# Optimization experiments

Hardware: AMD Instinct MI355X
Metric: run time of the kernel (lower is better)

Reference implementation:

```python
import jax, jax.numpy as jnp
import numpy as np

B, S, W = 128, 100, 20
D, L, H, DFF = 192, 6, 8, 256
DH = D // H

def _ln(x, g, b, eps=1e-5):
    m = jnp.mean(x, -1, keepdims=True)
    v = jnp.var(x, -1, keepdims=True)
    return (x - m) * jax.lax.rsqrt(v + eps) * g + b

def _pos_encoding(seq_len, d):
    pos = np.arange(seq_len, dtype=np.float32)[:, None]
    div = np.exp(np.arange(0, d, 2, dtype=np.float32) * (-np.log(10000.0) / d))
    pe = np.zeros((seq_len, d), dtype=np.float32)
    pe[:, 0::2] = np.sin(pos * div)
    pe[:, 1::2] = np.cos(pos * div)
    return jnp.asarray(pe)

def setup_inputs() -> dict:
    key = jax.random.key(0)
    ks = iter(jax.random.split(key, 80))
    def nrm(shape, s=0.05):
        return jax.random.normal(next(ks), shape, jnp.float32) * s
    inp = {
        'title_idx': jax.random.randint(next(ks), (B, S, W), 0, 1000),
        'class_idx': jax.random.randint(next(ks), (B, S, W), 0, 500),
        'process_idx': jax.random.randint(next(ks), (B, S, W), 0, 1000),
        'activity_type': jax.random.randint(next(ks), (B, S), 0, 4),
        'mouse_pos': jax.random.uniform(next(ks), (B, S, 2), jnp.float32),
        'rect': jax.random.uniform(next(ks), (B, S, W, 4), jnp.float32),
        'flags': jax.random.uniform(next(ks), (B, S, W, 2), jnp.float32),
        'keyboard_active': jax.random.uniform(next(ks), (B, S, 1), jnp.float32),
        'window_mask': jnp.ones((B, S, W), jnp.float32),
        'noise': jax.random.normal(next(ks), (W, B, D), jnp.float32),
        'title_emb': nrm((1000, 32)),
        'class_emb': nrm((500, 32)),
        'process_emb': nrm((1000, 32)),
        'spatial_w1': nrm((64, 6)), 'spatial_b1': nrm((64,)),
        'spatial_w2': nrm((32, 64)), 'spatial_b2': nrm((32,)),
        'wfuse_w': nrm((128, 128)), 'wfuse_b': nrm((128,)),
        'mouse_w1': nrm((32, 2)), 'mouse_b1': nrm((32,)),
        'mouse_w2': nrm((32, 32)), 'mouse_b2': nrm((32,)),
        'act_emb': nrm((4, 16)),
        'kbd_w': nrm((16, 1)), 'kbd_b': nrm((16,)),
        'afuse_w': nrm((64, 64)), 'afuse_b': nrm((64,)),
        'qkv_w': nrm((L, 3 * D, D)), 'qkv_b': nrm((L, 3 * D)),
        'out_w': nrm((L, D, D)), 'out_b': nrm((L, D)),
        'ff1_w': nrm((L, DFF, D)), 'ff1_b': nrm((L, DFF)),
        'ff2_w': nrm((L, D, DFF)), 'ff2_b': nrm((L, D)),
        'ln1_g': 1.0 + nrm((L, D)), 'ln1_b': nrm((L, D)),
        'ln2_g': 1.0 + nrm((L, D)), 'ln2_b': nrm((L, D)),
        'proj_w1': nrm((256, 192)), 'proj_b1': nrm((256,)),
        'proj_w2': nrm((4, 256)), 'proj_b2': nrm((4,)),
        'ex_w1': nrm((128, 192)), 'ex_b1': nrm((128,)),
        'ex_w2': nrm((1, 128)), 'ex_b2': nrm((1,)),
    }
    return inp

def reference(title_idx, class_idx, process_idx, activity_type, mouse_pos, rect, flags, keyboard_active, window_mask, noise, title_emb, class_emb, process_emb, spatial_w1, spatial_b1, spatial_w2, spatial_b2, wfuse_w, wfuse_b, mouse_w1, mouse_b1, mouse_w2, mouse_b2, act_emb, kbd_w, kbd_b, afuse_w, afuse_b, qkv_w, qkv_b, out_w, out_b, ff1_w, ff1_b, ff2_w, ff2_b, ln1_g, ln1_b, ln2_g, ln2_b, proj_w1, proj_b1, proj_w2, proj_b2, ex_w1, ex_b1, ex_w2, ex_b2):
    # ---- window feature extraction (vectorized over B,S,W) ----
    t = title_emb[title_idx]              # [B,S,W,32]
    c = class_emb[class_idx]
    p = process_emb[process_idx]
    sp_in = jnp.concatenate([rect, flags], -1)  # [B,S,W,6]
    sp = jax.nn.relu(sp_in @ spatial_w1.T + spatial_b1) @ spatial_w2.T + spatial_b2
    wcomb = jnp.concatenate([t, c, p, sp], -1)  # [B,S,W,128]
    wf = jax.nn.relu(wcomb @ wfuse_w.T + wfuse_b) * window_mask[..., None]
    avg_w = jnp.sum(wf, 2) / W            # mean over max_windows incl zero padding
    # ---- activity feature extraction ----
    mp = mouse_pos / jnp.array([1920.0, 1080.0], jnp.float32)
    mf = jax.nn.relu(mp @ mouse_w1.T + mouse_b1) @ mouse_w2.T + mouse_b2  # [B,S,32]
    ae = act_emb[activity_type]           # [B,S,16]
    kf = keyboard_active @ kbd_w.T + kbd_b  # [B,S,16]
    af = jax.nn.relu(jnp.concatenate([mf, ae, kf], -1) @ afuse_w.T + afuse_b)
    # ---- transformer ----
    x = jnp.concatenate([avg_w, af], -1) + _pos_encoding(S, D)[None]  # [B,S,192]
    scale = 1.0 / np.sqrt(DH)
    def block(h, prm):
        qw, qb, ow, ob, f1w, f1b, f2w, f2b, g1, b1, g2, b2 = prm
        qkv = h @ qw.T + qb
        q, k, v = jnp.split(qkv, 3, -1)
        q = q.reshape(B, S, H, DH); k = k.reshape(B, S, H, DH); v = v.reshape(B, S, H, DH)
        a = jax.nn.softmax(jnp.einsum('bqhd,bkhd->bhqk', q, k) * scale, -1)
        o = jnp.einsum('bhqk,bkhd->bqhd', a, v).reshape(B, S, D)
        h = _ln(h + o @ ow.T + ob, g1, b1)
        ff = jax.nn.relu(h @ f1w.T + f1b) @ f2w.T + f2b
        return _ln(h + ff, g2, b2), None
    x, _ = jax.lax.scan(block, x, (qkv_w, qkv_b, out_w, out_b, ff1_w, ff1_b, ff2_w, ff2_b, ln1_g, ln1_b, ln2_g, ln2_b))
    last = x[:, -1, :]                    # [B,192]
    # ---- per-slot heads (noise passed in deterministically) ----
    slot = last[None] + noise * 0.1       # [W,B,192]
    positions = jnp.transpose(jax.nn.relu(slot @ proj_w1.T + proj_b1) @ proj_w2.T + proj_b2, (1, 0, 2))  # [B,W,4]
    existence = jnp.transpose(jax.nn.sigmoid(jax.nn.relu(slot @ ex_w1.T + ex_b1) @ ex_w2.T + ex_b2)[..., 0], (1, 0))  # [B,W]
    return positions, existence
```

## Files before the change

### kernel.cpp

```cpp
#include <hip/hip_runtime.h>
#include <hip/hip_bf16.h>
#include <math.h>

#define B_ 128
#define S_ 100
#define W_ 20
#define D_ 192
#define L_ 6
#define H_ 8
#define DFF_ 256
#define DH_ 24
#define BS_ (B_*S_)
#define THREED_ 576

typedef short short8 __attribute__((ext_vector_type(8)));
typedef short short4v __attribute__((ext_vector_type(4)));
typedef float floatx16 __attribute__((ext_vector_type(16)));

__device__ __forceinline__ float posenc(int s, int c) {
  float freq = expf(-logf(10000.f) * (float)(2 * (c >> 1)) / (float)D_);
  float ang = (float)s * freq;
  return (c & 1) ? cosf(ang) : sinf(ang);
}

__device__ __forceinline__ short8 ld_frag8(const __hip_bfloat16* p) {
  short4v lo = *(const short4v*)p;
  short4v hi = *(const short4v*)(p + 4);
  short8 r;
  r[0]=lo[0]; r[1]=lo[1]; r[2]=lo[2]; r[3]=lo[3];
  r[4]=hi[0]; r[5]=hi[1]; r[6]=hi[2]; r[7]=hi[3];
  return r;
}

__device__ __forceinline__ short f2bf_s(float v) {
  __hip_bfloat16 t = __float2bfloat16(v);
  return *reinterpret_cast<short*>(&t);
}

__device__ __forceinline__ float dot4(float4 a, float4 b) {
  return a.x*b.x + a.y*b.y + a.z*b.z + a.w*b.w;
}

__global__ __launch_bounds__(256)
void convertprep_kernel(
    const float* __restrict__ s0, __hip_bfloat16* __restrict__ d0,
    const float* __restrict__ s1, __hip_bfloat16* __restrict__ d1,
    const float* __restrict__ s2, __hip_bfloat16* __restrict__ d2,
    const float* __restrict__ s3, __hip_bfloat16* __restrict__ d3,
    const float* __restrict__ te, const float* __restrict__ ce,
    const float* __restrict__ pe, const float* __restrict__ wfw,
    const float* __restrict__ wfb, const float* __restrict__ sw2,
    const float* __restrict__ sb2,
    float* __restrict__ TE2, float* __restrict__ CE2,
    float* __restrict__ PE2, __hip_bfloat16* __restrict__ WSPb,
    float* __restrict__ PEtab)
{
  int b = blockIdx.x, tid = threadIdx.x;
  if (b < 720) {
    const float* s; __hip_bfloat16* d; int base;
    if      (b < 324) { s = s0; d = d0; base = b; }
    else if (b < 432) { s = s1; d = d1; base = b - 324; }
    else if (b < 576) { s = s2; d = d2; base = b - 432; }
    else              { s = s3; d = d3; base = b - 576; }
    int i = (base * 256 + tid) * 8;
    float4 v0 = *(const float4*)(s + i);
    float4 v1 = *(const float4*)(s + i + 4);
    __hip_bfloat162* d2p = (__hip_bfloat162*)(d + i);
    d2p[0] = __float22bfloat162_rn(make_float2(v0.x, v0.y));
    d2p[1] = __float22bfloat162_rn(make_float2(v0.z, v0.w));
    d2p[2] = __float22bfloat162_rn(make_float2(v1.x, v1.y));
    d2p[3] = __float22bfloat162_rn(make_float2(v1.z, v1.w));
    return;
  }
  int blk = b - 720;
  if (blk < 1250) {
    int item = blk * 256 + tid;
    int v = item >> 7, o = item & 127;
    const float* src; float* dst; int base, vv;
    float a;
    if (v < 1000) {
      src = te; dst = TE2; base = 0; vv = v;
      a = wfb[o];
      const float4* w4 = (const float4*)(wfw + o * 128 + 96);
      const float4* b4 = (const float4*)sb2;
      #pragma unroll
      for (int k4 = 0; k4 < 8; ++k4) a += dot4(w4[k4], b4[k4]);
    } else if (v < 1500) {
      src = ce; dst = CE2; base = 32; vv = v - 1000; a = 0.f;
    } else {
      src = pe; dst = PE2; base = 64; vv = v - 1500; a = 0.f;
    }
    const float4* s4 = (const float4*)(src + vv * 32);
    const float4* w4 = (const float4*)(wfw + o * 128 + base);
    #pragma unroll
    for (int k4 = 0; k4 < 8; ++k4) a += dot4(s4[k4], w4[k4]);
    int op = ((o & 31) << 2) + (o >> 5);
    dst[vv * 128 + op] = a;
  } else if (blk < 1282) {
    int item = (blk - 1250) * 256 + tid;
    int j = item >> 7, o = item & 127;
    float a = 0.f;
    #pragma unroll 8
    for (int k = 0; k < 32; ++k) a += wfw[o * 128 + 96 + k] * sw2[k * 64 + j];
    WSPb[o * 64 + j] = __float2bfloat16(a);
  } else {
    int idx = (blk - 1282) * 256 + tid;
    int s_ = idx / D_, c = idx - s_ * D_;
    PEtab[idx] = posenc(s_, c);
  }
}

__global__ __launch_bounds__(512)
void encode8_kernel(
    const int* __restrict__ title_idx, const int* __restrict__ class_idx,
    const int* __restrict__ process_idx, const int* __restrict__ activity_type,
    const float* __restrict__ mouse_pos, const float* __restrict__ rect,
    const float* __restrict__ flags, const float* __restrict__ keyboard_active,
    const float* __restrict__ window_mask,
    const float* __restrict__ sw1, const float* __restrict__ sb1,
    const float* __restrict__ TE2, const float* __restrict__ CE2,
    const float* __restrict__ PE2, const __hip_bfloat16* __restrict__ WSPb,
    const float* __restrict__ PEtab,
    const float* __restrict__ mw1, const float* __restrict__ mb1,
    const float* __restrict__ mw2, const float* __restrict__ mb2,
    const float* __restrict__ act_emb, const float* __restrict__ kbw,
    const float* __restrict__ kbb,
    const float* __restrict__ afw, const float* __restrict__ afb,
    float* __restrict__ x, __hip_bfloat16* __restrict__ xb)
{
  __shared__ __hip_bfloat16 Bls[128][72];
  __shared__ int   idxS[8][20][3];
  __shared__ float maskS[8][20];
  __shared__ __align__(16) float rectS[8][20][8];

  int tid = threadIdx.x;
  int w = tid >> 6, lane = tid & 63;
  int m32 = lane & 31, half = lane >> 5;
  int bs0 = blockIdx.x * 8;
  int bs = bs0 + w;

  if (tid < 480) {
    int g2 = tid / 60, rem = tid % 60, which = rem / 20, w_ = rem % 20;
    const int* src = (which == 0) ? title_idx : (which == 1) ? class_idx : process_idx;
    idxS[g2][w_][which] = src[(bs0 + g2) * W_ + w_];
  }
  if (tid < 160) {
    int g2 = tid / 20, w_ = tid % 20;
    maskS[g2][w_] = window_mask[(bs0 + g2) * W_ + w_];
  }
  for (int e = tid; e < 960; e += 512) {
    int g2 = e / 120, rem = e % 120, w_ = rem / 6, c = rem % 6;
    int rg = (bs0 + g2) * W_ + w_;
    rectS[g2][w_][c] = (c < 4) ? rect[rg * 4 + c] : flags[rg * 2 + (c - 4)];
  }
  for (int e = tid; e < 1024; e += 512) {
    int col = e >> 3, k8 = e & 7;
    short8 v = *(const short8*)&WSPb[col * 64 + k8 * 8];
    *(short8*)&Bls[col][k8 * 8] = v;
  }
  __syncthreads();

  short8 afr[4];
  {
    float rc[6];
    bool act = (m32 < W_);
    if (act) {
      #pragma unroll
      for (int c = 0; c < 6; ++c) rc[c] = rectS[w][m32][c];
    }
    #pragma unroll
    for (int s = 0; s < 4; ++s) {
      short8 f;
      #pragma unroll
      for (int jp = 0; jp < 8; ++jp) {
        float a = 0.f;
        if (act) {
          int j = s * 16 + half * 8 + jp;
          const float* w1 = sw1 + j * 6;
          a = sb1[j];
          #pragma unroll
          for (int c = 0; c < 6; ++c) a += w1[c] * rc[c];
          a = fmaxf(a, 0.f);
        }
        f[jp] = f2bf_s(a);
      }
      afr[s] = f;
    }
  }

  floatx16 acc[4];
  #pragma unroll
  for (int nt = 0; nt < 4; ++nt)
    #pragma unroll
    for (int r = 0; r < 16; ++r) acc[nt][r] = 0.f;

  #pragma unroll
  for (int s = 0; s < 4; ++s) {
    int ko = s * 16 + half * 8;
    #pragma unroll
    for (int nt = 0; nt < 4; ++nt) {
      short8 bf = *(const short8*)&Bls[nt * 32 + m32][ko];
      acc[nt] = __builtin_amdgcn_mfma_f32_32x32x16_bf16(afr[s], bf, acc[nt], 0, 0, 0);
    }
  }

  float cs[4] = {0.f, 0.f, 0.f, 0.f};
  #pragma unroll
  for (int r = 0; r < 16; ++r) {
    int row = (r & 3) + 8 * (r >> 2) + 4 * half;
    if (row < W_) {
      int t  = idxS[w][row][0];
      int ci = idxS[w][row][1];
      int p  = idxS[w][row][2];
      float mk = maskS[w][row];
      float4 gt = *(const float4*)&TE2[(size_t)t  * 128 + m32 * 4];
      float4 gc = *(const float4*)&CE2[(size_t)ci * 128 + m32 * 4];
      float4 gp = *(const float4*)&PE2[(size_t)p  * 128 + m32 * 4];
      float g0 = gt.x + gc.x + gp.x;
      float g1 = gt.y + gc.y + gp.y;
      float g2v = gt.z + gc.z + gp.z;
      float g3 = gt.w + gc.w + gp.w;
      cs[0] += fmaxf(acc[0][r] + g0, 0.f) * mk;
      cs[1] += fmaxf(acc[1][r] + g1, 0.f) * mk;
      cs[2] += fmaxf(acc[2][r] + g2v, 0.f) * mk;
      cs[3] += fmaxf(acc[3][r] + g3, 0.f) * mk;
    }
  }
  #pragma unroll
  for (int nt = 0; nt < 4; ++nt) cs[nt] += __shfl_xor(cs[nt], 32);
  if (half == 0) {
    int s_ = bs % S_;
    #pragma unroll
    for (int nt = 0; nt < 4; ++nt) {
      int col = nt * 32 + m32;
      float v = cs[nt] * (1.f / (float)W_) + PEtab[s_ * D_ + col];
      x[(size_t)bs * D_ + col] = v;
      xb[(size_t)bs * D_ + col] = __float2bfloat16(v);
    }
  }

  {
    float* wsc = &rectS[w][0][0];
    if (lane < 32) {
      float mx = mouse_pos[bs * 2 + 0] * (1.f / 1920.f);
      float my = mouse_pos[bs * 2 + 1] * (1.f / 1080.f);
      wsc[64 + lane] = fmaxf(mw1[lane * 2] * mx + mw1[lane * 2 + 1] * my + mb1[lane], 0.f);
    }
    __builtin_amdgcn_wave_barrier();
    float cv;
    if (lane < 32) {
      float a = mb2[lane];
      const float4* wv = (const float4*)(mw2 + lane * 32);
      const float4* hv = (const float4*)(wsc + 64);
      #pragma unroll
      for (int k4 = 0; k4 < 8; ++k4) {
        float4 ww = wv[k4], hh = hv[k4];
        a += ww.x*hh.x + ww.y*hh.y + ww.z*hh.z + ww.w*hh.w;
      }
      cv = a;
    } else if (lane < 48) {
      cv = act_emb[activity_type[bs] * 16 + (lane - 32)];
    } else {
      cv = kbw[lane - 48] * keyboard_active[bs] + kbb[lane - 48];
    }
    wsc[lane] = cv;
    __builtin_amdgcn_wave_barrier();
    {
      float a = afb[lane];
      const float4* w4 = (const float4*)(afw + lane * 64);
      const float4* cp = (const float4*)wsc;
      #pragma unroll
      for (int k4 = 0; k4 < 16; ++k4) {
        float4 ww = w4[k4], c2 = cp[k4];
        a += ww.x*c2.x + ww.y*c2.y + ww.z*c2.z + ww.w*c2.w;
      }
      float v = fmaxf(a, 0.f);
      int cg = 128 + lane;
      float ovv = v + PEtab[(bs % S_) * D_ + cg];
      x[(size_t)bs * D_ + cg] = ovv;
      xb[(size_t)bs * D_ + cg] = __float2bfloat16(ovv);
    }
  }
}

__global__ __launch_bounds__(256)
void qkvattn_kernel(const __hip_bfloat16* __restrict__ xb,
                    const __hip_bfloat16* __restrict__ Wq,
                    const float* __restrict__ qb,
                    __hip_bfloat16* __restrict__ o)
{
  __shared__ __align__(16) char smem[40960];
  __hip_bfloat16* Asl = (__hip_bfloat16*)smem;
  __hip_bfloat16* Bsl = (__hip_bfloat16*)(smem + 18432);
  __hip_bfloat16* Qs  = (__hip_bfloat16*)smem;
  __hip_bfloat16* Ks  = (__hip_bfloat16*)(smem + 10240);
  __hip_bfloat16* Ps  = (__hip_bfloat16*)smem;
  __hip_bfloat16* Vt  = (__hip_bfloat16*)(smem + 33792);

  int bh = blockIdx.x;
  int hh = bh & 7, b = bh >> 3;
  int tid = threadIdx.x, lane = tid & 63, w = tid >> 6;
  int m32 = lane & 31, half = lane >> 5;

  for (int e = tid; e < (32 * 112) / 8; e += 256)
    ((float4*)Vt)[e] = make_float4(0.f, 0.f, 0.f, 0.f);

  int rA0 = tid >> 2,          hA0 = tid & 3;
  int rA1 = (tid + 256) >> 2,  hA1 = tid & 3;
  int rrA0 = rA0 < S_ ? rA0 : S_ - 1;
  int rrA1 = rA1 < S_ ? rA1 : S_ - 1;
  size_t baseA0 = (size_t)(b * S_ + rrA0) * D_;
  size_t baseA1 = (size_t)(b * S_ + rrA1) * D_;
  float4* dA0 = (float4*)&Asl[rA0 * 72 + hA0 * 16];
  float4* dA1 = (float4*)&Asl[rA1 * 72 + hA1 * 16];

  int rB0 = tid >> 2, hB0 = tid & 3;
  int tB0 = rB0 >> 5, jB0 = rB0 & 31;
  bool actB0 = (jB0 < DH_);
  bool isB1 = (tid < 128);
  int rB1 = (tid + 256) >> 2, hB1 = tid & 3;
  int tB1 = rB1 >> 5, jB1 = rB1 & 31;
  bool actB1 = isB1 && (jB1 < DH_);
  size_t baseB0 = actB0 ? (size_t)(tB0 * D_ + hh * DH_ + jB0) * D_ : 0;
  size_t baseB1 = actB1 ? (size_t)(tB1 * D_ + hh * DH_ + jB1) * D_ : 0;
  float4* dB0 = (float4*)&Bsl[rB0 * 72 + hB0 * 16];
  float4* dB1 = (float4*)&Bsl[rB1 * 72 + hB1 * 16];

  {
    float4 z = make_float4(0.f, 0.f, 0.f, 0.f);
    if (!actB0) { dB0[0] = z; dB0[1] = z; }
    if (isB1 && !actB1) { dB1[0] = z; dB1[1] = z; }
  }
  {
    const float4* s0 = (const float4*)&xb[baseA0 + hA0 * 16];
    float4 a00 = s0[0], a01 = s0[1];
    const float4* s1 = (const float4*)&xb[baseA1 + hA1 * 16];
    float4 a10 = s1[0], a11 = s1[1];
    if (actB0) {
      const float4* p = (const float4*)&Wq[baseB0 + hB0 * 16];
      dB0[0] = p[0]; dB0[1] = p[1];
    }
    if (actB1) {
      const float4* p = (const float4*)&Wq[baseB1 + hB1 * 16];
      dB1[0] = p[0]; dB1[1] = p[1];
    }
    dA0[0] = a00; dA0[1] = a01;
    dA1[0] = a10; dA1[1] = a11;
  }

  floatx16 acc[3];
  #pragma unroll
  for (int t = 0; t < 3; ++t)
    #pragma unroll
    for (int r = 0; r < 16; ++r) acc[t][r] = 0.f;

  for (int k0 = 0; k0 < D_; k0 += 64) {
    bool more = (k0 + 64 < D_);
    __syncthreads();
    float4 a00, a01, a10, a11, b00, b01, b10, b11;
    if (more) {
      const float4* s0 = (const float4*)&xb[baseA0 + k0 + 64 + hA0 * 16];
      a00 = s0[0]; a01 = s0[1];
      const float4* s1 = (const float4*)&xb[baseA1 + k0 + 64 + hA1 * 16];
      a10 = s1[0]; a11 = s1[1];
      if (actB0) {
        const float4* p = (const float4*)&Wq[baseB0 + k0 + 64 + hB0 * 16];
        b00 = p[0]; b01 = p[1];
      }
      if (actB1) {
        const float4* p = (const float4*)&Wq[baseB1 + k0 + 64 + hB1 * 16];
        b10 = p[0]; b11 = p[1];
      }
    }
    #pragma unroll
    for (int kc = 0; kc < 4; ++kc) {
      int ko = kc * 16 + half * 8;
      short8 a = *(const short8*)&Asl[(w * 32 + m32) * 72 + ko];
      #pragma unroll
      for (int t = 0; t < 3; ++t) {
        short8 bf = *(const short8*)&Bsl[(t * 32 + m32) * 72 + ko];
        acc[t] = __builtin_amdgcn_mfma_f32_32x32x16_bf16(a, bf, acc[t], 0, 0, 0);
      }
    }
    __syncthreads();
    if (more) {
      dA0[0] = a00; dA0[1] = a01;
      dA1[0] = a10; dA1[1] = a11;
      if (actB0) { dB0[0] = b00; dB0[1] = b01; }
      if (actB1) { dB1[0] = b10; dB1[1] = b11; }
    }
  }
  {
    bool dv = (m32 < DH_);
    float bq = dv ? qb[0 * D_ + hh * DH_ + m32] : 0.f;
    float bk = dv ? qb[1 * D_ + hh * DH_ + m32] : 0.f;
    float bv = dv ? qb[2 * D_ + hh * DH_ + m32] : 0.f;
    #pragma unroll
    for (int r = 0; r < 16; ++r) {
      int row = w * 32 + (r & 3) + 8 * (r >> 2) + 4 * half;
      Qs[row * 40 + m32] = __float2bfloat16(dv ? acc[0][r] + bq : 0.f);
      Ks[row * 40 + m32] = __float2bfloat16(dv ? acc[1][r] + bk : 0.f);
      if (dv && row < S_) Vt[m32 * 112 + row] = __float2bfloat16(acc[2][r] + bv);
    }
  }
  __syncthreads();

  floatx16 sc[4];
  #pragma unroll
  for (int nt = 0; nt < 4; ++nt)
    #pragma unroll
    for (int r = 0; r < 16; ++r) sc[nt][r] = 0.f;
  #pragma unroll
  for (int kc = 0; kc < 2; ++kc) {
    int ko = kc * 16 + half * 8;
    short8 a = *(const short8*)&Qs[(w * 32 + m32) * 40 + ko];
    #pragma unroll
    for (int nt = 0; nt < 4; ++nt) {
      short8 bf = *(const short8*)&Ks[(nt * 32 + m32) * 40 + ko];
      sc[nt] = __builtin_amdgcn_mfma_f32_32x32x16_bf16(a, bf, sc[nt], 0, 0, 0);
    }
  }
  __syncthreads();

  const float scale = 0.20412414523193154f;
  float rinv[16];
  #pragma unroll
  for (int r = 0; r < 16; ++r) {
    float mx = -1e30f;
    #pragma unroll
    for (int nt = 0; nt < 4; ++nt) {
      float s = sc[nt][r] * scale;
      if (nt == 3 && m32 >= 4) s = -1e30f;
      sc[nt][r] = s;
      mx = fmaxf(mx, s);
    }
    #pragma unroll
    for (int off = 1; off < 32; off <<= 1) mx = fmaxf(mx, __shfl_xor(mx, off));
    float sum = 0.f;
    #pragma unroll
    for (int nt = 0; nt < 4; ++nt) {
      float e = expf(sc[nt][r] - mx);
      sc[nt][r] = e;
      sum += e;
    }
    #pragma unroll
    for (int off = 1; off < 32; off <<= 1) sum += __shfl_xor(sum, off);
    rinv[r] = 1.f / sum;
  }
  #pragma unroll
  for (int r = 0; r < 16; ++r) {
    int rowl = (r & 3) + 8 * (r >> 2) + 4 * half;
    #pragma unroll
    for (int nt = 0; nt < 4; ++nt)
      Ps[(w * 32 + rowl) * 132 + nt * 32 + m32] = __float2bfloat16(sc[nt][r]);
  }

  floatx16 ov;
  #pragma unroll
  for (int r = 0; r < 16; ++r) ov[r] = 0.f;
  #pragma unroll
  for (int kt = 0; kt < 7; ++kt) {
    int ko = kt * 16 + half * 8;
    short8 a = ld_frag8(&Ps[(w * 32 + m32) * 132 + ko]);
    short8 bf = *(const short8*)&Vt[m32 * 112 + ko];
    ov = __builtin_amdgcn_mfma_f32_32x32x16_bf16(a, bf, ov, 0, 0, 0);
  }
  #pragma unroll
  for (int r = 0; r < 16; ++r) {
    int rowl = (r & 3) + 8 * (r >> 2) + 4 * half;
    int q = w * 32 + rowl;
    if (m32 < DH_ && q < S_)
      o[((size_t)(b * S_ + q)) * D_ + hh * DH_ + m32] =
          __float2bfloat16(ov[r] * rinv[r]);
  }
}

__global__ __launch_bounds__(256)
void outffln_kernel(const __hip_bfloat16* __restrict__ attb,
                    const __hip_bfloat16* __restrict__ Wo, const float* __restrict__ bo,
                    const float* __restrict__ g1, const float* __restrict__ b1v,
                    const __hip_bfloat16* __restrict__ W1, const float* __restrict__ b1,
                    const __hip_bfloat16* __restrict__ W2, const float* __restrict__ b2,
                    const float* __restrict__ g2, const float* __restrict__ b2v,
                    float* __restrict__ x, __hip_bfloat16* __restrict__ xb)
{
  __shared__ __align__(16) char arena[61952];
  __hip_bfloat16* AslA  = (__hip_bfloat16*)arena;
  __hip_bfloat16* BslA  = (__hip_bfloat16*)(arena + 9216);
  __hip_bfloat16* Afull = (__hip_bfloat16*)arena;
  __hip_bfloat16* BslB1 = (__hip_bfloat16*)(arena + 25088);
  __hip_bfloat16* C1    = (__hip_bfloat16*)arena;
  __hip_bfloat16* BslB2 = (__hip_bfloat16*)(arena + 33280);
  float (*psum)[2] = (float(*)[2])(arena + 60928);
  float (*psq)[2]  = (float(*)[2])(arena + 61440);

  int tid = threadIdx.x, lane = tid & 63, w = tid >> 6;
  int m32 = lane & 31, half = lane >> 5;
  int mt = w & 1, ng = w >> 1;
  int bm = blockIdx.x * 64;

  floatx16 accA[3];
  #pragma unroll
  for (int j = 0; j < 3; ++j)
    #pragma unroll
    for (int r = 0; r < 16; ++r) accA[j][r] = 0.f;

  {
    int ra = tid >> 2, ha = tid & 3;
    float4* dA = (float4*)&AslA[ra * 72 + ha * 16];
    int rb0 = tid >> 2,           hb0 = tid & 3;
    int rb1 = (tid + 256) >> 2,   hb1 = tid & 3;
    int rb2 = (tid + 512) >> 2,   hb2 = tid & 3;
    float4* dB0 = (float4*)&BslA[rb0 * 72 + hb0 * 16];
    float4* dB1 = (float4*)&BslA[rb1 * 72 + hb1 * 16];
    float4* dB2 = (float4*)&BslA[rb2 * 72 + hb2 * 16];

    {
      const float4* s = (const float4*)(attb + (size_t)(bm + ra) * D_ + ha * 16);
      dA[0] = s[0]; dA[1] = s[1];
      const float4* p0 = (const float4*)(Wo + (size_t)rb0 * D_ + hb0 * 16);
      dB0[0] = p0[0]; dB0[1] = p0[1];
      const float4* p1 = (const float4*)(Wo + (size_t)rb1 * D_ + hb1 * 16);
      dB1[0] = p1[0]; dB1[1] = p1[1];
      const float4* p2 = (const float4*)(Wo + (size_t)rb2 * D_ + hb2 * 16);
      dB2[0] = p2[0]; dB2[1] = p2[1];
    }
    for (int k0 = 0; k0 < D_; k0 += 64) {
      bool more = (k0 + 64 < D_);
      __syncthreads();
      float4 na0, na1, n00, n01, n10, n11, n20, n21;
      if (more) {
        const float4* s = (const float4*)(attb + (size_t)(bm + ra) * D_ + k0 + 64 + ha * 16);
        na0 = s[0]; na1 = s[1];
        const float4* p0 = (const float4*)(Wo + (size_t)rb0 * D_ + k0 + 64 + hb0 * 16);
        n00 = p0[0]; n01 = p0[1];
        const float4* p1 = (const float4*)(Wo + (size_t)rb1 * D_ + k0 + 64 + hb1 * 16);
        n10 = p1[0]; n11 = p1[1];
        const float4* p2 = (const float4*)(Wo + (size_t)rb2 * D_ + k0 + 64 + hb2 * 16);
        n20 = p2[0]; n21 = p2[1];
      }
      #pragma unroll
      for (int kc = 0; kc < 4; ++kc) {
        int ko = kc * 16 + half * 8;
        short8 a = *(const short8*)&AslA[(mt * 32 + m32) * 72 + ko];
        #pragma unroll
        for (int j = 0; j < 3; ++j) {
          short8 bf = *(const short8*)&BslA[((ng * 3 + j) * 32 + m32) * 72 + ko];
          accA[j] = __builtin_amdgcn_mfma_f32_32x32x16_bf16(a, bf, accA[j], 0, 0, 0);
        }
      }
      __syncthreads();
      if (more) {
        dA[0] = na0; dA[1] = na1;
        dB0[0] = n00; dB0[1] = n01;
        dB1[0] = n10; dB1[1] = n11;
        dB2[0] = n20; dB2[1] = n21;
      }
    }
  }
  {
    int rowb = mt * 32 + 4 * half;
    #pragma unroll
    for (int r = 0; r < 16; ++r) {
      int rl = rowb + (r & 3) + 8 * (r >> 2);
      int row = bm + rl;
      float p = 0.f;
      #pragma unroll
      for (int j = 0; j < 3; ++j) {
        int col = (ng * 3 + j) * 32 + m32;
        float t = accA[j][r] + bo[col] + x[(size_t)row * D_ + col];
        accA[j][r] = t;
        p += t;
      }
      #pragma unroll
      for (int off = 1; off < 32; off <<= 1) p += __shfl_xor(p, off);
      if (m32 == 0) psum[rl][ng] = p;
    }
    __syncthreads();
    float mean[16];
    #pragma unroll
    for (int r = 0; r < 16; ++r) {
      int rl = rowb + (r & 3) + 8 * (r >> 2);
      mean[r] = (psum[rl][0] + psum[rl][1]) * (1.f / (float)D_);
    }
    #pragma unroll
    for (int r = 0; r < 16; ++r) {
      int rl = rowb + (r & 3) + 8 * (r >> 2);
      float s = 0.f;
      #pragma unroll
      for (int j = 0; j < 3; ++j) { float dd = accA[j][r] - mean[r]; s += dd * dd; }
      #pragma unroll
      for (int off = 1; off < 32; off <<= 1) s += __shfl_xor(s, off);
      if (m32 == 0) psq[rl][ng] = s;
    }
    __syncthreads();
    #pragma unroll
    for (int r = 0; r < 16; ++r) {
      int rl = rowb + (r & 3) + 8 * (r >> 2);
      int row = bm + rl;
      float inv = rsqrtf((psq[rl][0] + psq[rl][1]) * (1.f / (float)D_) + 1e-5f);
      #pragma unroll
      for (int j = 0; j < 3; ++j) {
        int col = (ng * 3 + j) * 32 + m32;
        float ovv = (accA[j][r] - mean[r]) * inv * g1[col] + b1v[col];
        x[(size_t)row * D_ + col] = ovv;
        __hip_bfloat16 hb = __float2bfloat16(ovv);
        xb[(size_t)row * D_ + col] = hb;
        Afull[rl * 196 + col] = hb;
      }
    }
  }
  __syncthreads();

  floatx16 acc1[4];
  #pragma unroll
  for (int j = 0; j < 4; ++j)
    #pragma unroll
    for (int r = 0; r < 16; ++r) acc1[j][r] = 0.f;

  {
    int rb0 = tid >> 2,          hb0 = tid & 3;
    int rb1 = (tid + 256) >> 2,  hb1 = tid & 3;
    int rb2 = (tid + 512) >> 2,  hb2 = tid & 3;
    int rb3 = (tid + 768) >> 2,  hb3 = tid & 3;
    float4* dB0 = (float4*)&BslB1[rb0 * 72 + hb0 * 16];
    float4* dB1 = (float4*)&BslB1[rb1 * 72 + hb1 * 16];
    float4* dB2 = (float4*)&BslB1[rb2 * 72 + hb2 * 16];
    float4* dB3 = (float4*)&BslB1[rb3 * 72 + hb3 * 16];
    {
      const float4* p0 = (const float4*)(W1 + (size_t)rb0 * D_ + hb0 * 16);
      dB0[0] = p0[0]; dB0[1] = p0[1];
      const float4* p1 = (const float4*)(W1 + (size_t)rb1 * D_ + hb1 * 16);
      dB1[0] = p1[0]; dB1[1] = p1[1];
      const float4* p2 = (const float4*)(W1 + (size_t)rb2 * D_ + hb2 * 16);
      dB2[0] = p2[0]; dB2[1] = p2[1];
      const float4* p3 = (const float4*)(W1 + (size_t)rb3 * D_ + hb3 * 16);
      dB3[0] = p3[0]; dB3[1] = p3[1];
    }
    for (int k0 = 0; k0 < D_; k0 += 64) {
      bool more = (k0 + 64 < D_);
      __syncthreads();
      float4 n00, n01, n10, n11, n20, n21, n30, n31;
      if (more) {
        const float4* p0 = (const float4*)(W1 + (size_t)rb0 * D_ + k0 + 64 + hb0 * 16);
        n00 = p0[0]; n01 = p0[1];
        const float4* p1 = (const float4*)(W1 + (size_t)rb1 * D_ + k0 + 64 + hb1 * 16);
        n10 = p1[0]; n11 = p1[1];
        const float4* p2 = (const float4*)(W1 + (size_t)rb2 * D_ + k0 + 64 + hb2 * 16);
        n20 = p2[0]; n21 = p2[1];
        const float4* p3 = (const float4*)(W1 + (size_t)rb3 * D_ + k0 + 64 + hb3 * 16);
        n30 = p3[0]; n31 = p3[1];
      }
      #pragma unroll
      for (int kc = 0; kc < 4; ++kc) {
        int ko = kc * 16 + half * 8;
        short8 a = ld_frag8(&Afull[(mt * 32 + m32) * 196 + k0 + ko]);
        #pragma unroll
        for (int j = 0; j < 4; ++j) {
          short8 bf = *(const short8*)&BslB1[((ng * 4 + j) * 32 + m32) * 72 + ko];
          acc1[j] = __builtin_amdgcn_mfma_f32_32x32x16_bf16(a, bf, acc1[j], 0, 0, 0);
        }
      }
      __syncthreads();
      if (more) {
        dB0[0] = n00; dB0[1] = n01;
        dB1[0] = n10; dB1[1] = n11;
        dB2[0] = n20; dB2[1] = n21;
        dB3[0] = n30; dB3[1] = n31;
      }
    }
  }
  {
    int rowb = mt * 32 + 4 * half;
    #pragma unroll
    for (int j = 0; j < 4; ++j) {
      int col = (ng * 4 + j) * 32 + m32;
      float cb = b1[col];
      #pragma unroll
      for (int r = 0; r < 16; ++r) {
        int row = rowb + (r & 3) + 8 * (r >> 2);
        C1[row * 260 + col] = __float2bfloat16(fmaxf(acc1[j][r] + cb, 0.f));
      }
    }
  }

  floatx16 acc2[3];
  #pragma unroll
  for (int j = 0; j < 3; ++j)
    #pragma unroll
    for (int r = 0; r < 16; ++r) acc2[j][r] = 0.f;

  {
    int rb0 = tid >> 2,          hb0 = tid & 3;
    int rb1 = (tid + 256) >> 2,  hb1 = tid & 3;
    int rb2 = (tid + 512) >> 2,  hb2 = tid & 3;
    float4* dB0 = (float4*)&BslB2[rb0 * 72 + hb0 * 16];
    float4* dB1 = (float4*)&BslB2[rb1 * 72 + hb1 * 16];
    float4* dB2 = (float4*)&BslB2[rb2 * 72 + hb2 * 16];
    {
      const float4* p0 = (const float4*)(W2 + (size_t)rb0 * DFF_ + hb0 * 16);
      dB0[0] = p0[0]; dB0[1] = p0[1];
      const float4* p1 = (const float4*)(W2 + (size_t)rb1 * DFF_ + hb1 * 16);
      dB1[0] = p1[0]; dB1[1] = p1[1];
      const float4* p2 = (const float4*)(W2 + (size_t)rb2 * DFF_ + hb2 * 16);
      dB2[0] = p2[0]; dB2[1] = p2[1];
    }
    for (int k0 = 0; k0 < DFF_; k0 += 64) {
      bool more = (k0 + 64 < DFF_);
      __syncthreads();
      float4 n00, n01, n10, n11, n20, n21;
      if (more) {
        const float4* p0 = (const float4*)(W2 + (size_t)rb0 * DFF_ + k0 + 64 + hb0 * 16);
        n00 = p0[0]; n01 = p0[1];
        const float4* p1 = (const float4*)(W2 + (size_t)rb1 * DFF_ + k0 + 64 + hb1 * 16);
        n10 = p1[0]; n11 = p1[1];
        const float4* p2 = (const float4*)(W2 + (size_t)rb2 * DFF_ + k0 + 64 + hb2 * 16);
        n20 = p2[0]; n21 = p2[1];
      }
      #pragma unroll
      for (int kc = 0; kc < 4; ++kc) {
        int ko = kc * 16 + half * 8;
        short8 a = ld_frag8(&C1[(mt * 32 + m32) * 260 + k0 + ko]);
        #pragma unroll
        for (int j = 0; j < 3; ++j) {
          short8 bf = *(const short8*)&BslB2[((ng * 3 + j) * 32 + m32) * 72 + ko];
          acc2[j] = __builtin_amdgcn_mfma_f32_32x32x16_bf16(a, bf, acc2[j], 0, 0, 0);
        }
      }
      __syncthreads();
      if (more) {
        dB0[0] = n00; dB0[1] = n01;
        dB1[0] = n10; dB1[1] = n11;
        dB2[0] = n20; dB2[1] = n21;
      }
    }
  }

  int rowb = mt * 32 + 4 * half;
  #pragma unroll
  for (int r = 0; r < 16; ++r) {
    int rl = rowb + (r & 3) + 8 * (r >> 2);
    int row = bm + rl;
    float p = 0.f;
    #pragma unroll
    for (int j = 0; j < 3; ++j) {
      int col = (ng * 3 + j) * 32 + m32;
      float t = acc2[j][r] + b2[col] + x[(size_t)row * D_ + col];
      acc2[j][r] = t;
      p += t;
    }
    #pragma unroll
    for (int off = 1; off < 32; off <<= 1) p += __shfl_xor(p, off);
    if (m32 == 0) psum[rl][ng] = p;
  }
  __syncthreads();
  float mean[16];
  #pragma unroll
  for (int r = 0; r < 16; ++r) {
    int rl = rowb + (r & 3) + 8 * (r >> 2);
    mean[r] = (psum[rl][0] + psum[rl][1]) * (1.f / (float)D_);
  }
  #pragma unroll
  for (int r = 0; r < 16; ++r) {
    int rl = rowb + (r & 3) + 8 * (r >> 2);
    float s = 0.f;
    #pragma unroll
    for (int j = 0; j < 3; ++j) { float dd = acc2[j][r] - mean[r]; s += dd * dd; }
    #pragma unroll
    for (int off = 1; off < 32; off <<= 1) s += __shfl_xor(s, off);
    if (m32 == 0) psq[rl][ng] = s;
  }
  __syncthreads();
  #pragma unroll
  for (int r = 0; r < 16; ++r) {
    int rl = rowb + (r & 3) + 8 * (r >> 2);
    int row = bm + rl;
    float inv = rsqrtf((psq[rl][0] + psq[rl][1]) * (1.f / (float)D_) + 1e-5f);
    #pragma unroll
    for (int j = 0; j < 3; ++j) {
      int col = (ng * 3 + j) * 32 + m32;
      float ovv = (acc2[j][r] - mean[r]) * inv * g2[col] + b2v[col];
      x[(size_t)row * D_ + col] = ovv;
      xb[(size_t)row * D_ + col] = __float2bfloat16(ovv);
    }
  }
}

__global__ __launch_bounds__(256)
void head3_kernel(const float* __restrict__ x, const float* __restrict__ noise,
                  const float* __restrict__ pw1, const float* __restrict__ pb1,
                  const float* __restrict__ pw2, const float* __restrict__ pb2,
                  const float* __restrict__ ew1, const float* __restrict__ eb1,
                  const float* __restrict__ ew2, const float* __restrict__ eb2,
                  float* __restrict__ out)
{
  __shared__ float slotS[4][192];
  __shared__ float phS[4][256];
  __shared__ float ehS[4][128];
  int blk = blockIdx.x;
  int b = blk / 5, g = blk - b * 5;
  int tid = threadIdx.x;

  const float* lastrow = x + ((size_t)b * S_ + (S_ - 1)) * D_;
  for (int e = tid; e < 4 * 192; e += 256) {
    int wl = e / 192, c = e - wl * 192;
    int wg = g * 4 + wl;
    slotS[wl][c] = lastrow[c] + noise[((size_t)wg * B_ + b) * D_ + c] * 0.1f;
  }
  __syncthreads();

  bool doe = (tid < 128);
  float accp[4], acce[4];
  {
    float bp = pb1[tid];
    float be = doe ? eb1[tid] : 0.f;
    #pragma unroll
    for (int wl = 0; wl < 4; ++wl) { accp[wl] = bp; acce[wl] = be; }
  }
  {
    const float4* wr = (const float4*)(pw1 + (size_t)tid * D_);
    const float4* we = (const float4*)(ew1 + (size_t)(doe ? tid : 0) * D_);
    for (int k4 = 0; k4 < 48; ++k4) {
      float4 wv = wr[k4];
      float4 ev = we[k4];
      #pragma unroll
      for (int wl = 0; wl < 4; ++wl) {
        float4 sv = *(const float4*)&slotS[wl][k4 * 4];
        accp[wl] += wv.x*sv.x + wv.y*sv.y + wv.z*sv.z + wv.w*sv.w;
        if (doe) acce[wl] += ev.x*sv.x + ev.y*sv.y + ev.z*sv.z + ev.w*sv.w;
      }
    }
  }
  #pragma unroll
  for (int wl = 0; wl < 4; ++wl) {
    phS[wl][tid] = fmaxf(accp[wl], 0.f);
    if (doe) ehS[wl][tid] = fmaxf(acce[wl], 0.f);
  }
  __syncthreads();

  if (tid < 16) {
    int wl = tid >> 2, c = tid & 3;
    float a = pb2[c];
    const float4* wr = (const float4*)(pw2 + c * 256);
    const float4* pp = (const float4*)&phS[wl][0];
    for (int k = 0; k < 64; ++k) {
      float4 wv = wr[k], pv = pp[k];
      a += wv.x*pv.x + wv.y*pv.y + wv.z*pv.z + wv.w*pv.w;
    }
    out[((size_t)b * W_ + g * 4 + wl) * 4 + c] = a;
  } else if (tid >= 64 && tid < 68) {
    int wl = tid - 64;
    float a = eb2[0];
    const float4* wr = (const float4*)ew2;
    const float4* pp = (const float4*)&ehS[wl][0];
    for (int k = 0; k < 32; ++k) {
      float4 wv = wr[k], pv = pp[k];
      a += wv.x*pv.x + wv.y*pv.y + wv.z*pv.z + wv.w*pv.w;
    }
    out[(size_t)B_ * W_ * 4 + (size_t)b * W_ + g * 4 + wl] = 1.f / (1.f + expf(-a));
  }
}

extern "C" void kernel_launch(void* const* d_in, const int* in_sizes, int n_in,
                              void* d_out, int out_size, void* d_ws, size_t ws_size,
                              hipStream_t stream)
{
  const int*   title_idx       = (const int*)  d_in[0];
  const int*   class_idx       = (const int*)  d_in[1];
  const int*   process_idx     = (const int*)  d_in[2];
  const int*   activity_type   = (const int*)  d_in[3];
  const float* mouse_pos       = (const float*)d_in[4];
  const float* rect            = (const float*)d_in[5];
  const float* flags           = (const float*)d_in[6];
  const float* keyboard_active = (const float*)d_in[7];
  const float* window_mask     = (const float*)d_in[8];
  const float* noise           = (const float*)d_in[9];
  const float* title_emb       = (const float*)d_in[10];
  const float* class_emb       = (const float*)d_in[11];
  const float* process_emb     = (const float*)d_in[12];
  const float* spatial_w1      = (const float*)d_in[13];
  const float* spatial_b1      = (const float*)d_in[14];
  const float* spatial_w2      = (const float*)d_in[15];
  const float* spatial_b2      = (const float*)d_in[16];
  const float* wfuse_w         = (const float*)d_in[17];
  const float* wfuse_b         = (const float*)d_in[18];
  const float* mouse_w1        = (const float*)d_in[19];
  const float* mouse_b1        = (const float*)d_in[20];
  const float* mouse_w2        = (const float*)d_in[21];
  const float* mouse_b2        = (const float*)d_in[22];
  const float* act_emb         = (const float*)d_in[23];
  const float* kbd_w           = (const float*)d_in[24];
  const float* kbd_b           = (const float*)d_in[25];
  const float* afuse_w         = (const float*)d_in[26];
  const float* afuse_b         = (const float*)d_in[27];
  const float* qkv_w           = (const float*)d_in[28];
  const float* qkv_b           = (const float*)d_in[29];
  const float* out_w           = (const float*)d_in[30];
  const float* out_b           = (const float*)d_in[31];
  const float* ff1_w           = (const float*)d_in[32];
  const float* ff1_b           = (const float*)d_in[33];
  const float* ff2_w           = (const float*)d_in[34];
  const float* ff2_b           = (const float*)d_in[35];
  const float* ln1_g           = (const float*)d_in[36];
  const float* ln1_b           = (const float*)d_in[37];
  const float* ln2_g           = (const float*)d_in[38];
  const float* ln2_b           = (const float*)d_in[39];
  const float* proj_w1         = (const float*)d_in[40];
  const float* proj_b1         = (const float*)d_in[41];
  const float* proj_w2         = (const float*)d_in[42];
  const float* proj_b2         = (const float*)d_in[43];
  const float* ex_w1           = (const float*)d_in[44];
  const float* ex_b1           = (const float*)d_in[45];
  const float* ex_w2           = (const float*)d_in[46];
  const float* ex_b2           = (const float*)d_in[47];

  float* out = (float*)d_out;

  float* x = (float*)d_ws;
  __hip_bfloat16* xb   = (__hip_bfloat16*)(x + (size_t)BS_ * D_);
  __hip_bfloat16* attb = xb   + (size_t)BS_ * D_;
  __hip_bfloat16* wqb  = attb + (size_t)BS_ * D_;
  __hip_bfloat16* wob  = wqb  + (size_t)L_ * THREED_ * D_;
  __hip_bfloat16* wf1b = wob  + (size_t)L_ * D_ * D_;
  __hip_bfloat16* wf2b = wf1b + (size_t)L_ * DFF_ * D_;
  float* TE2  = (float*)(wf2b + (size_t)L_ * D_ * DFF_);
  float* CE2  = TE2  + 1000 * 128;
  float* PE2  = CE2  + 500 * 128;
  __hip_bfloat16* WSPb = (__hip_bfloat16*)(PE2 + 1000 * 128);
  float* PEtab = (float*)(WSPb + 128 * 64);
  (void)ws_size; (void)n_in; (void)in_sizes; (void)out_size;

  convertprep_kernel<<<2077, 256, 0, stream>>>(
      qkv_w, wqb, out_w, wob, ff1_w, wf1b, ff2_w, wf2b,
      title_emb, class_emb, process_emb, wfuse_w, wfuse_b,
      spatial_w2, spatial_b2, TE2, CE2, PE2, WSPb, PEtab);

  encode8_kernel<<<BS_ / 8, 512, 0, stream>>>(
      title_idx, class_idx, process_idx, activity_type, mouse_pos, rect, flags,
      keyboard_active, window_mask, spatial_w1, spatial_b1,
      TE2, CE2, PE2, WSPb, PEtab,
      mouse_w1, mouse_b1, mouse_w2, mouse_b2, act_emb, kbd_w, kbd_b,
      afuse_w, afuse_b, x, xb);

  for (int l = 0; l < L_; ++l) {
    qkvattn_kernel<<<B_ * H_, 256, 0, stream>>>(
        xb, wqb + (size_t)l * THREED_ * D_, qkv_b + (size_t)l * THREED_, attb);
    outffln_kernel<<<BS_ / 64, 256, 0, stream>>>(
        attb, wob + (size_t)l * D_ * D_, out_b + (size_t)l * D_,
        ln1_g + (size_t)l * D_, ln1_b + (size_t)l * D_,
        wf1b + (size_t)l * DFF_ * D_, ff1_b + (size_t)l * DFF_,
        wf2b + (size_t)l * D_ * DFF_, ff2_b + (size_t)l * D_,
        ln2_g + (size_t)l * D_, ln2_b + (size_t)l * D_, x, xb);
  }

  head3_kernel<<<B_ * 5, 256, 0, stream>>>(
      x, noise, proj_w1, proj_b1, proj_w2, proj_b2,
      ex_w1, ex_b1, ex_w2, ex_b2, out);
}
```

Before: 657.0 us.

## Widen out-proj K tile to 96 and keep residuals in registers

The out-projection GEMM in the fused out/FF/LN kernel now stages 96-wide K chunks (two iterations instead of three), with a new staging index map and a padded LDS stride of 104. The residual x values are prefetched into registers before the GEMM, and the post-LN1 values are kept in registers for the second residual, so the later global reads of x go away. This cuts barrier rounds and global traffic but adds many live registers (96 floats), which risks spills or lower occupancy.

Result: faster. 637.5 us (-3.0%).

```diff
diff --git a/kernel.cpp b/kernel.cpp
--- a/kernel.cpp
+++ b/kernel.cpp
@@ -486,7 +486,7 @@
 {
   __shared__ __align__(16) char arena[61952];
   __hip_bfloat16* AslA  = (__hip_bfloat16*)arena;
-  __hip_bfloat16* BslA  = (__hip_bfloat16*)(arena + 9216);
+  __hip_bfloat16* BslA  = (__hip_bfloat16*)(arena + 13312);
   __hip_bfloat16* Afull = (__hip_bfloat16*)arena;
   __hip_bfloat16* BslB1 = (__hip_bfloat16*)(arena + 25088);
   __hip_bfloat16* C1    = (__hip_bfloat16*)arena;
@@ -505,56 +505,102 @@
     #pragma unroll
     for (int r = 0; r < 16; ++r) accA[j][r] = 0.f;
 
-  {
-    int ra = tid >> 2, ha = tid & 3;
-    float4* dA = (float4*)&AslA[ra * 72 + ha * 16];
-    int rb0 = tid >> 2,           hb0 = tid & 3;
-    int rb1 = (tid + 256) >> 2,   hb1 = tid & 3;
-    int rb2 = (tid + 512) >> 2,   hb2 = tid & 3;
-    float4* dB0 = (float4*)&BslA[rb0 * 72 + hb0 * 16];
-    float4* dB1 = (float4*)&BslA[rb1 * 72 + hb1 * 16];
-    float4* dB2 = (float4*)&BslA[rb2 * 72 + hb2 * 16];
+  float xres[3][16];
+  {
+    int rowb0 = mt * 32 + 4 * half;
+    #pragma unroll
+    for (int r = 0; r < 16; ++r) {
+      int rl = rowb0 + (r & 3) + 8 * (r >> 2);
+      #pragma unroll
+      for (int j = 0; j < 3; ++j)
+        xres[j][r] = x[(size_t)(bm + rl) * D_ + (ng * 3 + j) * 32 + m32];
+    }
+  }
+  float h1v[3][16];
+
+  {
+    int eA0 = tid;           int rA0 = eA0 / 6, hA0 = eA0 % 6;
+    bool sA1 = (tid < 128);
+    int eA1 = tid + 256;     int rA1 = eA1 / 6, hA1 = eA1 % 6;
+    float4* dA0 = (float4*)&AslA[rA0 * 104 + hA0 * 16];
+    float4* dA1 = (float4*)&AslA[rA1 * 104 + hA1 * 16];
+
+    int eB0 = tid;           int rb0 = eB0 / 6, hb0 = eB0 % 6;
+    int eB1 = tid + 256;     int rb1 = eB1 / 6, hb1 = eB1 % 6;
+    int eB2 = tid + 512;     int rb2 = eB2 / 6, hb2 = eB2 % 6;
+    int eB3 = tid + 768;     int rb3 = eB3 / 6, hb3 = eB3 % 6;
+    bool sB4 = (tid < 128);
+    int eB4 = tid + 1024;    int rb4 = eB4 / 6, hb4 = eB4 % 6;
+    float4* dB0 = (float4*)&BslA[rb0 * 104 + hb0 * 16];
+    float4* dB1 = (float4*)&BslA[rb1 * 104 + hb1 * 16];
+    float4* dB2 = (float4*)&BslA[rb2 * 104 + hb2 * 16];
+    float4* dB3 = (float4*)&BslA[rb3 * 104 + hb3 * 16];
+    float4* dB4 = (float4*)&BslA[rb4 * 104 + hb4 * 16];
 
     {
-      const float4* s = (const float4*)(attb + (size_t)(bm + ra) * D_ + ha * 16);
-      dA[0] = s[0]; dA[1] = s[1];
+      const float4* s0 = (const float4*)(attb + (size_t)(bm + rA0) * D_ + hA0 * 16);
+      dA0[0] = s0[0]; dA0[1] = s0[1];
+      if (sA1) {
+        const float4* s1 = (const float4*)(attb + (size_t)(bm + rA1) * D_ + hA1 * 16);
+        dA1[0] = s1[0]; dA1[1] = s1[1];
+      }
       const float4* p0 = (const float4*)(Wo + (size_t)rb0 * D_ + hb0 * 16);
       dB0[0] = p0[0]; dB0[1] = p0[1];
       const float4* p1 = (const float4*)(Wo + (size_t)rb1 * D_ + hb1 * 16);
       dB1[0] = p1[0]; dB1[1] = p1[1];
       const float4* p2 = (const float4*)(Wo + (size_t)rb2 * D_ + hb2 * 16);
       dB2[0] = p2[0]; dB2[1] = p2[1];
-    }
-    for (int k0 = 0; k0 < D_; k0 += 64) {
-      bool more = (k0 + 64 < D_);
+      const float4* p3 = (const float4*)(Wo + (size_t)rb3 * D_ + hb3 * 16);
+      dB3[0] = p3[0]; dB3[1] = p3[1];
+      if (sB4) {
+        const float4* p4 = (const float4*)(Wo + (size_t)rb4 * D_ + hb4 * 16);
+        dB4[0] = p4[0]; dB4[1] = p4[1];
+      }
+    }
+    for (int k0 = 0; k0 < D_; k0 += 96) {
+      bool more = (k0 + 96 < D_);
       __syncthreads();
-      float4 na0, na1, n00, n01, n10, n11, n20, n21;
+      float4 a00, a01, a10, a11;
+      float4 n00, n01, n10, n11, n20, n21, n30, n31, n40, n41;
       if (more) {
-        const float4* s = (const float4*)(attb + (size_t)(bm + ra) * D_ + k0 + 64 + ha * 16);
-        na0 = s[0]; na1 = s[1];
-        const float4* p0 = (const float4*)(Wo + (size_t)rb0 * D_ + k0 + 64 + hb0 * 16);
+        const float4* s0 = (const float4*)(attb + (size_t)(bm + rA0) * D_ + k0 + 96 + hA0 * 16);
+        a00 = s0[0]; a01 = s0[1];
+        if (sA1) {
+          const float4* s1 = (const float4*)(attb + (size_t)(bm + rA1) * D_ + k0 + 96 + hA1 * 16);
+          a10 = s1[0]; a11 = s1[1];
+        }
+        const float4* p0 = (const float4*)(Wo + (size_t)rb0 * D_ + k0 + 96 + hb0 * 16);
         n00 = p0[0]; n01 = p0[1];
-        const float4* p1 = (const float4*)(Wo + (size_t)rb1 * D_ + k0 + 64 + hb1 * 16);
+        const float4* p1 = (const float4*)(Wo + (size_t)rb1 * D_ + k0 + 96 + hb1 * 16);
         n10 = p1[0]; n11 = p1[1];
-        const float4* p2 = (const float4*)(Wo + (size_t)rb2 * D_ + k0 + 64 + hb2 * 16);
+        const float4* p2 = (const float4*)(Wo + (size_t)rb2 * D_ + k0 + 96 + hb2 * 16);
         n20 = p2[0]; n21 = p2[1];
-      }
-      #pragma unroll
-      for (int kc = 0; kc < 4; ++kc) {
+        const float4* p3 = (const float4*)(Wo + (size_t)rb3 * D_ + k0 + 96 + hb3 * 16);
+        n30 = p3[0]; n31 = p3[1];
+        if (sB4) {
+          const float4* p4 = (const float4*)(Wo + (size_t)rb4 * D_ + k0 + 96 + hb4 * 16);
+          n40 = p4[0]; n41 = p4[1];
+        }
+      }
+      #pragma unroll
+      for (int kc = 0; kc < 6; ++kc) {
         int ko = kc * 16 + half * 8;
-        short8 a = *(const short8*)&AslA[(mt * 32 + m32) * 72 + ko];
+        short8 a = *(const short8*)&AslA[(mt * 32 + m32) * 104 + ko];
         #pragma unroll
         for (int j = 0; j < 3; ++j) {
-          short8 bf = *(const short8*)&BslA[((ng * 3 + j) * 32 + m32) * 72 + ko];
+          short8 bf = *(const short8*)&BslA[((ng * 3 + j) * 32 + m32) * 104 + ko];
           accA[j] = __builtin_amdgcn_mfma_f32_32x32x16_bf16(a, bf, accA[j], 0, 0, 0);
         }
       }
       __syncthreads();
       if (more) {
-        dA[0] = na0; dA[1] = na1;
+        dA0[0] = a00; dA0[1] = a01;
+        if (sA1) { dA1[0] = a10; dA1[1] = a11; }
         dB0[0] = n00; dB0[1] = n01;
         dB1[0] = n10; dB1[1] = n11;
         dB2[0] = n20; dB2[1] = n21;
+        dB3[0] = n30; dB3[1] = n31;
+        if (sB4) { dB4[0] = n40; dB4[1] = n41; }
       }
     }
   }
@@ -563,12 +609,11 @@
     #pragma unroll
     for (int r = 0; r < 16; ++r) {
       int rl = rowb + (r & 3) + 8 * (r >> 2);
-      int row = bm + rl;
       float p = 0.f;
       #pragma unroll
       for (int j = 0; j < 3; ++j) {
         int col = (ng * 3 + j) * 32 + m32;
-        float t = accA[j][r] + bo[col] + x[(size_t)row * D_ + col];
+        float t = accA[j][r] + bo[col] + xres[j][r];
         accA[j][r] = t;
         p += t;
       }
@@ -603,6 +648,7 @@
       for (int j = 0; j < 3; ++j) {
         int col = (ng * 3 + j) * 32 + m32;
         float ovv = (accA[j][r] - mean[r]) * inv * g1[col] + b1v[col];
+        h1v[j][r] = ovv;
         x[(size_t)row * D_ + col] = ovv;
         __hip_bfloat16 hb = __float2bfloat16(ovv);
         xb[(size_t)row * D_ + col] = hb;
@@ -740,12 +786,11 @@
   #pragma unroll
   for (int r = 0; r < 16; ++r) {
     int rl = rowb + (r & 3) + 8 * (r >> 2);
-    int row = bm + rl;
     float p = 0.f;
     #pragma unroll
     for (int j = 0; j < 3; ++j) {
       int col = (ng * 3 + j) * 32 + m32;
-      float t = acc2[j][r] + b2[col] + x[(size_t)row * D_ + col];
+      float t = acc2[j][r] + b2[col] + h1v[j][r];
       acc2[j][r] = t;
       p += t;
     }
```
